# Kernel tuning notes

Measured on AMD Instinct MI355X. Metric: run time of the kernel, lower is better.

The kernel has to match this reference:

```python
import jax, jax.numpy as jnp
import numpy as np

TOP_K = 2
LORA_SCALE = 32.0 / 16.0  # alpha / r


def setup_inputs() -> dict:
    key = jax.random.key(0)
    ks = jax.random.split(key, 11)
    B, S, D, F, E, R = 4, 1024, 2048, 5632, 8, 16
    sd, sf = 1.0 / np.sqrt(D), 1.0 / np.sqrt(F)
    return {
        "x": jax.random.normal(ks[0], (B, S, D), jnp.float32),
        "gate_w": jax.random.normal(ks[1], (E, D), jnp.float32) * 0.02,
        "w1": jax.random.normal(ks[2], (F, D), jnp.float32) * sd,
        "w3": jax.random.normal(ks[3], (F, D), jnp.float32) * sd,
        "w2": jax.random.normal(ks[4], (D, F), jnp.float32) * sf,
        "a1": jax.random.normal(ks[5], (E, R, D), jnp.float32) * sd,
        "b1": jax.random.normal(ks[6], (E, F, R), jnp.float32) * 0.01,
        "a3": jax.random.normal(ks[7], (E, R, D), jnp.float32) * sd,
        "b3": jax.random.normal(ks[8], (E, F, R), jnp.float32) * 0.01,
        "a2": jax.random.normal(ks[9], (E, R, F), jnp.float32) * sf,
        "b2": jax.random.normal(ks[10], (E, D, R), jnp.float32) * 0.01,
    }


def reference(x, gate_w, w1, w3, w2, a1, b1, a3, b3, a2, b2):
    B, S, D = x.shape
    E = gate_w.shape[0]
    xf = x.reshape(B * S, D)                      # [N, D] tokens
    N = xf.shape[0]

    # Mixtral-style router: top-k over expert logits, softmax over selected.
    logits = xf @ gate_w.T                        # [N, E]
    top_w, top_i = jax.lax.top_k(logits, TOP_K)   # [N, k]
    routing = jax.nn.softmax(top_w, axis=-1)
    # Dense [N, E] routing-weight matrix (zero for unselected experts).
    w_full = jnp.zeros((N, E), x.dtype).at[jnp.arange(N)[:, None], top_i].add(routing)

    # Shared base up-projections computed once (same for every expert).
    base1 = xf @ w1.T                             # [N, F]
    base3 = xf @ w3.T                             # [N, F]

    def expert_step(acc, p):
        A1, B1, A3, B3, A2, B2, we = p            # we: [N] routing weight
        h1 = base1 + ((xf @ A1.T) @ B1.T) * LORA_SCALE
        h3 = base3 + ((xf @ A3.T) @ B3.T) * LORA_SCALE
        act = jax.nn.silu(h1) * h3                # SwiGLU, per-expert
        out = act @ w2.T + ((act @ A2.T) @ B2.T) * LORA_SCALE
        return acc + we[:, None] * out, None

    init = jnp.zeros((N, D), x.dtype)
    out, _ = jax.lax.scan(expert_step, init, (a1, b1, a3, b3, a2, b2, w_full.T))
    return out.reshape(B, S, D)
```

## Files before the change

### kernel.cpp

```cpp
#include <hip/hip_runtime.h>
#include <stdint.h>

#define NTOK 4096
#define DDIM 2048
#define FDIM 5632
#define NEXP 8
#define RLORA 16
#define TWOF 11264
#define BCOLS 11520
#define PADROWS 10240
#define LSCALE 2.0f

typedef __attribute__((ext_vector_type(4))) float f32x4;
typedef __attribute__((ext_vector_type(8))) short short8;
typedef unsigned short u16;

#define AS1 __attribute__((address_space(1)))
#define AS3 __attribute__((address_space(3)))

__device__ __forceinline__ float b2f(short s) {
  union { float f; unsigned u; } v;
  v.u = ((unsigned)(u16)s) << 16;
  return v.f;
}
__device__ __forceinline__ u16 f2b(float f) {
  union { float f; unsigned u; } v; v.f = f;
  unsigned r = v.u + 0x7fffu + ((v.u >> 16) & 1u);
  return (u16)(r >> 16);
}

__global__ __launch_bounds__(256) void cast_kernel(const float* __restrict__ src, u16* __restrict__ dst, int n4) {
  int stride = gridDim.x * 256;
  for (int i = blockIdx.x * 256 + threadIdx.x; i < n4; i += stride) {
    float4 v = reinterpret_cast<const float4*>(src)[i];
    ushort4 o;
    o.x = f2b(v.x); o.y = f2b(v.y); o.z = f2b(v.z); o.w = f2b(v.w);
    reinterpret_cast<ushort4*>(dst)[i] = o;
  }
}

__global__ __launch_bounds__(256) void cast_ball(const float* __restrict__ w1, const float* __restrict__ w3,
                                                 const float* __restrict__ a1, const float* __restrict__ a3,
                                                 u16* __restrict__ Ball) {
  const int n4 = BCOLS * DDIM / 4;
  int stride = gridDim.x * 256;
  for (int i = blockIdx.x * 256 + threadIdx.x; i < n4; i += stride) {
    int row = i >> 9;
    int c4 = i & 511;
    const float* src;
    if (row < FDIM)            src = w1 + (size_t)row * DDIM;
    else if (row < TWOF)       src = w3 + (size_t)(row - FDIM) * DDIM;
    else if (row < TWOF + 128) src = a1 + (size_t)(row - TWOF) * DDIM;
    else                       src = a3 + (size_t)(row - TWOF - 128) * DDIM;
    float4 v = reinterpret_cast<const float4*>(src)[c4];
    ushort4 o;
    o.x = f2b(v.x); o.y = f2b(v.y); o.z = f2b(v.z); o.w = f2b(v.w);
    reinterpret_cast<ushort4*>(Ball)[i] = o;
  }
}

__global__ __launch_bounds__(256) void router_cast(const float* __restrict__ x, const float* __restrict__ gw,
                                                   int2* __restrict__ tok_e, float2* __restrict__ tok_w,
                                                   u16* __restrict__ xb) {
  int tok = blockIdx.x;
  const float* xr = x + (size_t)tok * DDIM;
  int j0 = threadIdx.x * 8;
  float4 v0 = *reinterpret_cast<const float4*>(xr + j0);
  float4 v1 = *reinterpret_cast<const float4*>(xr + j0 + 4);
  float v[8] = {v0.x, v0.y, v0.z, v0.w, v1.x, v1.y, v1.z, v1.w};
  short8 ob;
#pragma unroll
  for (int j = 0; j < 8; ++j) ob[j] = (short)f2b(v[j]);
  *reinterpret_cast<short8*>(xb + (size_t)tok * DDIM + j0) = ob;
  float acc[NEXP];
#pragma unroll
  for (int e = 0; e < NEXP; ++e) {
    const float* gr = gw + e * DDIM + j0;
    float s = 0.f;
#pragma unroll
    for (int j = 0; j < 8; ++j) s += v[j] * gr[j];
    acc[e] = s;
  }
#pragma unroll
  for (int e = 0; e < NEXP; ++e) {
#pragma unroll
    for (int off = 32; off > 0; off >>= 1) acc[e] += __shfl_down(acc[e], off);
  }
  __shared__ float red[4][NEXP];
  int wid = threadIdx.x >> 6;
  int lane = threadIdx.x & 63;
  if (lane == 0) {
#pragma unroll
    for (int e = 0; e < NEXP; ++e) red[wid][e] = acc[e];
  }
  __syncthreads();
  if (threadIdx.x == 0) {
    float l[NEXP];
#pragma unroll
    for (int e = 0; e < NEXP; ++e) l[e] = red[0][e] + red[1][e] + red[2][e] + red[3][e];
    int i0 = 0;
#pragma unroll
    for (int e = 1; e < NEXP; ++e) if (l[e] > l[i0]) i0 = e;
    int i1 = (i0 == 0) ? 1 : 0;
#pragma unroll
    for (int e = 0; e < NEXP; ++e) if (e != i0 && e != i1 && l[e] > l[i1]) i1 = e;
    float ex = __expf(l[i1] - l[i0]);
    float w0 = 1.f / (1.f + ex);
    float w1v = ex / (1.f + ex);
    int2 ev; ev.x = i0; ev.y = i1;
    float2 wv; wv.x = w0; wv.y = w1v;
    tok_e[tok] = ev;
    tok_w[tok] = wv;
  }
}

__global__ __launch_bounds__(256) void build_pairs(const int2* __restrict__ tok_e,
                                                   int* __restrict__ pair_tok,
                                                   int* __restrict__ pair_k, int* __restrict__ poff) {
  __shared__ int cnt[NEXP];
  __shared__ int base[NEXP + 1];
  __shared__ int cur[NEXP];
  if (threadIdx.x < NEXP) cnt[threadIdx.x] = 0;
  __syncthreads();
  for (int t = threadIdx.x; t < NTOK; t += 256) {
    int2 ee = tok_e[t];
    atomicAdd(&cnt[ee.x], 1);
    atomicAdd(&cnt[ee.y], 1);
  }
  for (int i = threadIdx.x; i < PADROWS; i += 256) pair_tok[i] = -1;
  __syncthreads();
  if (threadIdx.x == 0) {
    int o = 0;
#pragma unroll
    for (int e = 0; e < NEXP; ++e) { base[e] = o; o += ((cnt[e] + 255) >> 8) << 8; }
    base[NEXP] = o;
  }
  __syncthreads();
  if (threadIdx.x < NEXP) cur[threadIdx.x] = base[threadIdx.x];
  __syncthreads();
  for (int t = threadIdx.x; t < NTOK; t += 256) {
    int2 ee = tok_e[t];
    int s0 = atomicAdd(&cur[ee.x], 1);
    pair_tok[s0] = t; pair_k[s0] = 0;
    int s1 = atomicAdd(&cur[ee.y], 1);
    pair_tok[s1] = t; pair_k[s1] = 1;
  }
  __syncthreads();
  if (threadIdx.x <= NEXP) poff[threadIdx.x] = base[threadIdx.x];
}

__device__ __forceinline__ void stage64(const u16* __restrict__ src, int ld, char* ldsb, int tid) {
#pragma unroll
  for (int h = 0; h < 4; ++h) {
    int q = h * 256 + tid;
    int r = q >> 3, g = q & 7;
    int gs = g ^ (r & 7);
    const char* s = (const char*)(src + (size_t)r * ld) + gs * 16;
    __builtin_amdgcn_global_load_lds((const AS1 void*)s, (AS3 void*)(ldsb + q * 16), 16, 0, 0);
  }
}

__device__ __forceinline__ void mm128(const u16* __restrict__ A, const u16* __restrict__ B,
                                      int lda, int ldb, int NT,
                                      char* lA, char* lB, int tid,
                                      int rowAb, int rowBb, int col0,
                                      f32x4 (&acc)[4][4]) {
  for (int t = 0; t < NT; ++t) {
    __syncthreads();
    stage64(A + (size_t)t * 64, lda, lA, tid);
    stage64(B + (size_t)t * 64, ldb, lB, tid);
    __syncthreads();
    short8 av[4], bv[4];
#pragma unroll
    for (int kh = 0; kh < 2; ++kh) {
      int col = col0 ^ (kh << 6);
#pragma unroll
      for (int i = 0; i < 4; ++i) {
        av[i] = *(const short8*)(lA + rowAb + i * 2048 + col);
        bv[i] = *(const short8*)(lB + rowBb + i * 2048 + col);
      }
#pragma unroll
      for (int i = 0; i < 4; ++i)
#pragma unroll
        for (int j = 0; j < 4; ++j)
          acc[i][j] = __builtin_amdgcn_mfma_f32_16x16x32_bf16(av[i], bv[j], acc[i][j], 0, 0, 0);
    }
  }
}

__global__ __launch_bounds__(256, 4) void gemm_base(const u16* __restrict__ xb, const u16* __restrict__ Ball,
                                                    u16* __restrict__ base13) {
  __shared__ char lA[16384];
  __shared__ char lB[16384];
  const int tid = threadIdx.x;
  const int lane = tid & 63, wid = tid >> 6;
  const int wr = wid >> 1, wc = wid & 1;
  const int lm = lane & 15, lg = lane >> 4;
  const int col0 = (lg << 4) ^ ((lm & 7) << 4);
  const int rowAb = (wr * 64 + lm) * 128;
  const int rowBb = (wc * 64 + lm) * 128;
  const int lq = (lane >> 4) << 2;
  int orig = blockIdx.x;
  int wgid = (orig & 7) * 360 + (orig >> 3);
  int mi = wgid & 31, nt = wgid >> 5;
  int m0 = mi << 7, n0 = nt << 7;
  f32x4 acc[4][4];
  f32x4 z = {0.f, 0.f, 0.f, 0.f};
#pragma unroll
  for (int i = 0; i < 4; ++i)
#pragma unroll
    for (int j = 0; j < 4; ++j) acc[i][j] = z;
  mm128(xb + (size_t)m0 * DDIM, Ball + (size_t)n0 * DDIM, DDIM, DDIM, DDIM / 64,
        lA, lB, tid, rowAb, rowBb, col0, acc);
#pragma unroll
  for (int i = 0; i < 4; ++i) {
#pragma unroll
    for (int n = 0; n < 4; ++n) {
      int col = n0 + wc * 64 + n * 16 + lm;
#pragma unroll
      for (int q = 0; q < 4; ++q) {
        int row = m0 + wr * 64 + i * 16 + lq + q;
        base13[(size_t)row * BCOLS + col] = f2b(acc[i][n][q]);
      }
    }
  }
}

__global__ __launch_bounds__(256) void act_kernel(const u16* __restrict__ base13,
                                                  const float* __restrict__ b1, const float* __restrict__ b3,
                                                  const int* __restrict__ pair_tok, const int* __restrict__ poff,
                                                  u16* __restrict__ act) {
  __shared__ float lb1[128 * 16];
  __shared__ float lb3[128 * 16];
  int f0 = blockIdx.x * 128;
  int r0 = blockIdx.y * 32;
  if (r0 >= poff[NEXP]) return;
  int e = 0;
  while (r0 >= poff[e + 1]) ++e;
  const float4* pb1 = reinterpret_cast<const float4*>(b1 + ((size_t)e * FDIM + f0) * RLORA);
  const float4* pb3 = reinterpret_cast<const float4*>(b3 + ((size_t)e * FDIM + f0) * RLORA);
  for (int i = threadIdx.x; i < 128 * 16 / 4; i += 256) {
    int r = i >> 2, c = i & 3;
    int cs = (c + (r >> 5)) & 3;
    *reinterpret_cast<float4*>(lb1 + r * 16 + cs * 4) = pb1[i];
    *reinterpret_cast<float4*>(lb3 + r * 16 + cs * 4) = pb3[i];
  }
  __syncthreads();
  int pr = r0 + (threadIdx.x >> 3);
  int fg = (threadIdx.x & 7) << 4;
  int tok = pair_tok[pr];
  if (tok < 0) return;
  const u16* bp = base13 + (size_t)tok * BCOLS;
  short8 x1a = *(const short8*)(bp + TWOF + e * 16);
  short8 x1b = *(const short8*)(bp + TWOF + e * 16 + 8);
  short8 x3a = *(const short8*)(bp + TWOF + NEXP * RLORA + e * 16);
  short8 x3b = *(const short8*)(bp + TWOF + NEXP * RLORA + e * 16 + 8);
  float xa1[16], xa3[16];
#pragma unroll
  for (int r = 0; r < 8; ++r) {
    xa1[r] = b2f(x1a[r]); xa1[r + 8] = b2f(x1b[r]);
    xa3[r] = b2f(x3a[r]); xa3[r + 8] = b2f(x3b[r]);
  }
  short8 h1a = *(const short8*)(bp + f0 + fg);
  short8 h1b = *(const short8*)(bp + f0 + fg + 8);
  short8 h3a = *(const short8*)(bp + FDIM + f0 + fg);
  short8 h3b = *(const short8*)(bp + FDIM + f0 + fg + 8);
  short8 o0, o1;
#pragma unroll
  for (int ii = 0; ii < 16; ++ii) {
    float hb1 = b2f(ii < 8 ? h1a[ii] : h1b[ii - 8]);
    float hb3 = b2f(ii < 8 ? h3a[ii] : h3b[ii - 8]);
    int row = fg + ii;
    int rot = row >> 5;
    const float* l1 = lb1 + row * 16;
    const float* l3 = lb3 + row * 16;
    float d1 = 0.f, d3 = 0.f;
#pragma unroll
    for (int c = 0; c < 4; ++c) {
      int cs = ((c + rot) & 3) << 2;
      float4 v1 = *reinterpret_cast<const float4*>(l1 + cs);
      float4 v3 = *reinterpret_cast<const float4*>(l3 + cs);
      d1 += xa1[4 * c + 0] * v1.x + xa1[4 * c + 1] * v1.y + xa1[4 * c + 2] * v1.z + xa1[4 * c + 3] * v1.w;
      d3 += xa3[4 * c + 0] * v3.x + xa3[4 * c + 1] * v3.y + xa3[4 * c + 2] * v3.z + xa3[4 * c + 3] * v3.w;
    }
    float h1 = hb1 + LSCALE * d1;
    float h3 = hb3 + LSCALE * d3;
    float s = h1 / (1.f + __expf(-h1));
    u16 ob = f2b(s * h3);
    if (ii < 8) o0[ii] = (short)ob; else o1[ii - 8] = (short)ob;
  }
  short8* dst = (short8*)(act + (size_t)pr * FDIM + f0 + fg);
  dst[0] = o0;
  dst[1] = o1;
}

__global__ __launch_bounds__(256) void ya2_kernel(const u16* __restrict__ act, const u16* __restrict__ a2b,
                                                  const int* __restrict__ poff, float* __restrict__ ya2) {
  __shared__ char lA[8192];
  __shared__ char lB[2048];
  int m0 = blockIdx.x * 64;
  if (m0 >= poff[NEXP]) return;
  int e = 0;
  while (m0 >= poff[e + 1]) ++e;
  int f0 = blockIdx.y * (FDIM / 2);
  const int tid = threadIdx.x;
  const int lane = tid & 63, w = tid >> 6;
  const int lm = lane & 15, lg = lane >> 4;
  const int col0 = (lg << 4) ^ ((lm & 7) << 4);
  const int rowAb = (w * 16 + lm) * 128;
  const int rowBb = lm * 128;
  const int lq = (lane >> 4) << 2;
  const u16* A = act + (size_t)m0 * FDIM + f0;
  const u16* B = a2b + (size_t)e * RLORA * FDIM + f0;
  f32x4 acc = {0.f, 0.f, 0.f, 0.f};
  for (int t = 0; t < FDIM / 128; ++t) {
    __syncthreads();
#pragma unroll
    for (int h = 0; h < 2; ++h) {
      int q = h * 256 + tid, r = q >> 3, g = q & 7, gs = g ^ (r & 7);
      const char* s = (const char*)(A + (size_t)t * 64 + (size_t)r * FDIM) + gs * 16;
      __builtin_amdgcn_global_load_lds((const AS1 void*)s, (AS3 void*)(lA + q * 16), 16, 0, 0);
    }
    if (tid < 128) {
      int q = tid, r = q >> 3, g = q & 7, gs = g ^ (r & 7);
      const char* s = (const char*)(B + (size_t)t * 64 + (size_t)r * FDIM) + gs * 16;
      __builtin_amdgcn_global_load_lds((const AS1 void*)s, (AS3 void*)(lB + q * 16), 16, 0, 0);
    }
    __syncthreads();
#pragma unroll
    for (int kh = 0; kh < 2; ++kh) {
      int col = col0 ^ (kh << 6);
      short8 av = *(const short8*)(lA + rowAb + col);
      short8 bv = *(const short8*)(lB + rowBb + col);
      acc = __builtin_amdgcn_mfma_f32_16x16x32_bf16(av, bv, acc, 0, 0, 0);
    }
  }
#pragma unroll
  for (int q = 0; q < 4; ++q)
    atomicAdd(&ya2[(size_t)(m0 + w * 16 + lq + q) * RLORA + lm], acc[q]);
}

__global__ __launch_bounds__(256, 4) void gemm_down(const u16* __restrict__ act, const u16* __restrict__ w2b,
                                                    const float* __restrict__ b2, const float* __restrict__ ya2,
                                                    const int* __restrict__ pair_tok, const int* __restrict__ pair_k,
                                                    const int* __restrict__ poff,
                                                    float* __restrict__ slots) {
  int orig = blockIdx.x;
  int wgid = (orig & 7) * 160 + (orig >> 3);
  int nt = wgid & 15;
  int miL = wgid >> 4;
  int mi = ((miL % 10) << 3) + (miL / 10);
  int m0 = mi << 7;
  if (m0 >= poff[NEXP]) return;
  int e = 0;
  while (m0 >= poff[e + 1]) ++e;
  int n0 = nt << 7;
  __shared__ char lA[16384];
  __shared__ char lB[16384];
  const int tid = threadIdx.x;
  const int lane = tid & 63, wid = tid >> 6;
  const int wr = wid >> 1, wc = wid & 1;
  const int lm = lane & 15, lg = lane >> 4;
  const int col0 = (lg << 4) ^ ((lm & 7) << 4);
  const int rowAb = (wr * 64 + lm) * 128;
  const int rowBb = (wc * 64 + lm) * 128;
  const int lq = (lane >> 4) << 2;
  f32x4 acc[4][4];
  f32x4 z = {0.f, 0.f, 0.f, 0.f};
#pragma unroll
  for (int i = 0; i < 4; ++i)
#pragma unroll
    for (int j = 0; j < 4; ++j) acc[i][j] = z;
  mm128(act + (size_t)m0 * FDIM, w2b + (size_t)n0 * FDIM, FDIM, FDIM, FDIM / 64,
        lA, lB, tid, rowAb, rowBb, col0, acc);
#pragma unroll
  for (int n = 0; n < 4; ++n) {
    int col = n0 + wc * 64 + n * 16 + lm;
    const float* b2p = b2 + ((size_t)e * DDIM + col) * RLORA;
    float b2v[16];
#pragma unroll
    for (int rr = 0; rr < 16; ++rr) b2v[rr] = b2p[rr];
#pragma unroll
    for (int i = 0; i < 4; ++i) {
#pragma unroll
      for (int q = 0; q < 4; ++q) {
        int pidx = m0 + wr * 64 + i * 16 + lq + q;
        int tok = pair_tok[pidx];
        if (tok < 0) continue;
        const float* yr = ya2 + (size_t)pidx * RLORA;
        float dot = 0.f;
#pragma unroll
        for (int rr = 0; rr < 16; ++rr) dot += yr[rr] * b2v[rr];
        slots[((size_t)tok * 2 + pair_k[pidx]) * DDIM + col] = acc[i][n][q] + LSCALE * dot;
      }
    }
  }
}

__global__ __launch_bounds__(256) void combine_kernel(const float4* __restrict__ slots,
                                                      const float2* __restrict__ tok_w,
                                                      float4* __restrict__ out) {
  const int n4 = NTOK * (DDIM / 4);
  int stride = gridDim.x * 256;
  for (int i = blockIdx.x * 256 + threadIdx.x; i < n4; i += stride) {
    int tok = i >> 9;
    int c = i & 511;
    float2 w = tok_w[tok];
    float4 v0 = slots[(size_t)(tok * 2) * 512 + c];
    float4 v1 = slots[(size_t)(tok * 2 + 1) * 512 + c];
    float4 o;
    o.x = w.x * v0.x + w.y * v1.x;
    o.y = w.x * v0.y + w.y * v1.y;
    o.z = w.x * v0.z + w.y * v1.z;
    o.w = w.x * v0.w + w.y * v1.w;
    out[i] = o;
  }
}

extern "C" void kernel_launch(void* const* d_in, const int* in_sizes, int n_in,
                              void* d_out, int out_size, void* d_ws, size_t ws_size,
                              hipStream_t stream) {
  (void)in_sizes; (void)n_in; (void)out_size; (void)ws_size;
  const float* x  = (const float*)d_in[0];
  const float* gw = (const float*)d_in[1];
  const float* w1 = (const float*)d_in[2];
  const float* w3 = (const float*)d_in[3];
  const float* w2 = (const float*)d_in[4];
  const float* a1 = (const float*)d_in[5];
  const float* b1 = (const float*)d_in[6];
  const float* a3 = (const float*)d_in[7];
  const float* b3 = (const float*)d_in[8];
  const float* a2 = (const float*)d_in[9];
  const float* b2 = (const float*)d_in[10];
  float* out = (float*)d_out;

  char* ws = (char*)d_ws;
  size_t off = 0;
  auto take = [&](size_t bytes) -> char* {
    char* p = ws + off;
    off += (bytes + 255) & ~(size_t)255;
    return p;
  };
  char* reg1 = take((size_t)NTOK * BCOLS * 2);
  u16* base13 = (u16*)reg1;
  float* slots = (float*)reg1;
  char* reg2 = take((size_t)PADROWS * FDIM * 2);
  u16* actb = (u16*)reg2;
  u16* xb = (u16*)reg2;
  u16* Ball = (u16*)(reg2 + (size_t)NTOK * DDIM * 2);
  u16* w2b = (u16*)take((size_t)DDIM * FDIM * 2);
  u16* a2b = (u16*)take((size_t)NEXP * RLORA * FDIM * 2);
  float* ya2 = (float*)take((size_t)PADROWS * RLORA * 4);
  int2* tok_e   = (int2*)take((size_t)NTOK * 8);
  float2* tok_w = (float2*)take((size_t)NTOK * 8);
  int* pair_tok = (int*)take((size_t)PADROWS * 4);
  int* pair_k   = (int*)take((size_t)PADROWS * 4);
  int* poff     = (int*)take(256);

  cast_ball<<<2048, 256, 0, stream>>>(w1, w3, a1, a3, Ball);
  cast_kernel<<<1024, 256, 0, stream>>>(w2, w2b, DDIM * FDIM / 4);
  cast_kernel<<<64, 256, 0, stream>>>(a2, a2b, NEXP * RLORA * FDIM / 4);
  router_cast<<<NTOK, 256, 0, stream>>>(x, gw, tok_e, tok_w, xb);
  build_pairs<<<1, 256, 0, stream>>>(tok_e, pair_tok, pair_k, poff);
  gemm_base<<<2880, 256, 0, stream>>>(xb, Ball, base13);
  dim3 g3(FDIM / 128, PADROWS / 32);
  act_kernel<<<g3, 256, 0, stream>>>(base13, b1, b3, pair_tok, poff, actb);
  hipMemsetAsync(ya2, 0, (size_t)PADROWS * RLORA * 4, stream);
  dim3 gy(PADROWS / 64, 2);
  ya2_kernel<<<gy, 256, 0, stream>>>(actb, a2b, poff, ya2);
  gemm_down<<<1280, 256, 0, stream>>>(actb, w2b, b2, ya2, pair_tok, pair_k, poff, slots);
  combine_kernel<<<2048, 256, 0, stream>>>((const float4*)slots, tok_w, (float4*)out);
}
```

Measured before the change: 776.7 us.

## Fuse SwiGLU activation into base up-projection GEMM epilogue with interleaved w1/w3 tiles

Interleaves w1 and w3 rows in 64-row blocks so each 128-column tile of the base GEMM holds matching h1 and h3 columns. Adds an LDS exchange so the epilogue computes the LoRA correction, SiLU and product in place and writes bf16 activations straight to both expert slots. This removes the bf16 base13 round trip and the separate act_kernel. The x·A1/A3 LoRA projections move to a new per-expert xa_kernel, and B1/B3 are transposed to bf16. In exchange the epilogue runs on only half the waves, does scattered global writes, and uses more LDS per block, which may lower occupancy.

```diff
diff --git a/kernel.cpp b/kernel.cpp
--- a/kernel.cpp
+++ b/kernel.cpp
@@ -7,7 +7,6 @@
 #define NEXP 8
 #define RLORA 16
 #define TWOF 11264
-#define BCOLS 11520
 #define PADROWS 10240
 #define LSCALE 2.0f
 
@@ -39,23 +38,51 @@
   }
 }
 
-__global__ __launch_bounds__(256) void cast_ball(const float* __restrict__ w1, const float* __restrict__ w3,
-                                                 const float* __restrict__ a1, const float* __restrict__ a3,
-                                                 u16* __restrict__ Ball) {
-  const int n4 = BCOLS * DDIM / 4;
+__global__ __launch_bounds__(256) void cast_ball_i(const float* __restrict__ w1, const float* __restrict__ w3,
+                                                   u16* __restrict__ Ball) {
+  const int n4 = TWOF * DDIM / 4;
   int stride = gridDim.x * 256;
   for (int i = blockIdx.x * 256 + threadIdx.x; i < n4; i += stride) {
     int row = i >> 9;
     int c4 = i & 511;
-    const float* src;
-    if (row < FDIM)            src = w1 + (size_t)row * DDIM;
-    else if (row < TWOF)       src = w3 + (size_t)(row - FDIM) * DDIM;
-    else if (row < TWOF + 128) src = a1 + (size_t)(row - TWOF) * DDIM;
-    else                       src = a3 + (size_t)(row - TWOF - 128) * DDIM;
+    int blk = row >> 7, w = row & 127;
+    const float* src = (w < 64) ? (w1 + (size_t)(blk * 64 + w) * DDIM)
+                                : (w3 + (size_t)(blk * 64 + w - 64) * DDIM);
     float4 v = reinterpret_cast<const float4*>(src)[c4];
     ushort4 o;
     o.x = f2b(v.x); o.y = f2b(v.y); o.z = f2b(v.z); o.w = f2b(v.w);
     reinterpret_cast<ushort4*>(Ball)[i] = o;
+  }
+}
+
+__global__ __launch_bounds__(256) void cast_a13(const float* __restrict__ a1, const float* __restrict__ a3,
+                                                u16* __restrict__ a13b) {
+  const int n4 = 256 * DDIM / 4;
+  int stride = gridDim.x * 256;
+  for (int i = blockIdx.x * 256 + threadIdx.x; i < n4; i += stride) {
+    int row = i >> 9, c4 = i & 511;
+    int e = row >> 5, w = row & 31;
+    const float* src = (w < 16) ? (a1 + (size_t)(e * 16 + w) * DDIM)
+                                : (a3 + (size_t)(e * 16 + w - 16) * DDIM);
+    float4 v = reinterpret_cast<const float4*>(src)[c4];
+    ushort4 o;
+    o.x = f2b(v.x); o.y = f2b(v.y); o.z = f2b(v.z); o.w = f2b(v.w);
+    reinterpret_cast<ushort4*>(a13b)[i] = o;
+  }
+}
+
+__global__ __launch_bounds__(256) void cast_b13t(const float* __restrict__ b1, const float* __restrict__ b3,
+                                                 u16* __restrict__ b1t, u16* __restrict__ b3t) {
+  int e = blockIdx.y;
+  const int n4 = FDIM * RLORA / 4;
+  for (int i = blockIdx.x * 256 + threadIdx.x; i < n4; i += gridDim.x * 256) {
+    int f = i >> 2, r4 = (i & 3) << 2;
+    float4 v = *reinterpret_cast<const float4*>(b1 + ((size_t)e * FDIM + f) * RLORA + r4);
+    ushort4 o; o.x = f2b(v.x); o.y = f2b(v.y); o.z = f2b(v.z); o.w = f2b(v.w);
+    *reinterpret_cast<ushort4*>(b1t + ((size_t)f * NEXP + e) * RLORA + r4) = o;
+    v = *reinterpret_cast<const float4*>(b3 + ((size_t)e * FDIM + f) * RLORA + r4);
+    ushort4 o3; o3.x = f2b(v.x); o3.y = f2b(v.y); o3.z = f2b(v.z); o3.w = f2b(v.w);
+    *reinterpret_cast<ushort4*>(b3t + ((size_t)f * NEXP + e) * RLORA + r4) = o3;
   }
 }
 
@@ -116,7 +143,8 @@
 
 __global__ __launch_bounds__(256) void build_pairs(const int2* __restrict__ tok_e,
                                                    int* __restrict__ pair_tok,
-                                                   int* __restrict__ pair_k, int* __restrict__ poff) {
+                                                   int* __restrict__ pair_k, int* __restrict__ poff,
+                                                   int2* __restrict__ slot2) {
   __shared__ int cnt[NEXP];
   __shared__ int base[NEXP + 1];
   __shared__ int cur[NEXP];
@@ -144,6 +172,8 @@
     pair_tok[s0] = t; pair_k[s0] = 0;
     int s1 = atomicAdd(&cur[ee.y], 1);
     pair_tok[s1] = t; pair_k[s1] = 1;
+    int2 sv; sv.x = s0; sv.y = s1;
+    slot2[t] = sv;
   }
   __syncthreads();
   if (threadIdx.x <= NEXP) poff[threadIdx.x] = base[threadIdx.x];
@@ -188,10 +218,72 @@
   }
 }
 
-__global__ __launch_bounds__(256, 4) void gemm_base(const u16* __restrict__ xb, const u16* __restrict__ Ball,
-                                                    u16* __restrict__ base13) {
-  __shared__ char lA[16384];
-  __shared__ char lB[16384];
+__global__ __launch_bounds__(256) void xa_kernel(const u16* __restrict__ xb, const u16* __restrict__ a13b,
+                                                 const int* __restrict__ pair_tok, const int* __restrict__ poff,
+                                                 float* __restrict__ xa) {
+  __shared__ char lA[8192];
+  __shared__ char lB[4096];
+  int m0 = blockIdx.x * 64;
+  if (m0 >= poff[NEXP]) return;
+  int e = 0;
+  while (m0 >= poff[e + 1]) ++e;
+  const int tid = threadIdx.x;
+  const int lane = tid & 63, w = tid >> 6;
+  const int lm = lane & 15, lg = lane >> 4;
+  const int col0 = (lg << 4) ^ ((lm & 7) << 4);
+  const int rowAb = (w * 16 + lm) * 128;
+  const int rowB1 = lm * 128;
+  const int rowB3 = (16 + lm) * 128;
+  const int lq = lg << 2;
+  int r0 = tid >> 3;
+  int t0 = pair_tok[m0 + r0];      if (t0 < 0) t0 = 0;
+  int t1 = pair_tok[m0 + 32 + r0]; if (t1 < 0) t1 = 0;
+  const u16* B = a13b + (size_t)e * 32 * DDIM;
+  f32x4 acc0 = {0.f, 0.f, 0.f, 0.f}, acc1 = {0.f, 0.f, 0.f, 0.f};
+  for (int t = 0; t < DDIM / 64; ++t) {
+    __syncthreads();
+    {
+      int g = tid & 7, gs = g ^ (r0 & 7);
+      const char* s = (const char*)(xb + (size_t)t0 * DDIM + t * 64) + gs * 16;
+      __builtin_amdgcn_global_load_lds((const AS1 void*)s, (AS3 void*)(lA + tid * 16), 16, 0, 0);
+    }
+    {
+      int r = 32 + r0, g = tid & 7, gs = g ^ (r & 7);
+      const char* s = (const char*)(xb + (size_t)t1 * DDIM + t * 64) + gs * 16;
+      __builtin_amdgcn_global_load_lds((const AS1 void*)s, (AS3 void*)(lA + 4096 + tid * 16), 16, 0, 0);
+    }
+    {
+      int r = tid >> 3, g = tid & 7, gs = g ^ (r & 7);
+      const char* s = (const char*)(B + (size_t)r * DDIM + t * 64) + gs * 16;
+      __builtin_amdgcn_global_load_lds((const AS1 void*)s, (AS3 void*)(lB + tid * 16), 16, 0, 0);
+    }
+    __syncthreads();
+#pragma unroll
+    for (int kh = 0; kh < 2; ++kh) {
+      int col = col0 ^ (kh << 6);
+      short8 av = *(const short8*)(lA + rowAb + col);
+      short8 b1v = *(const short8*)(lB + rowB1 + col);
+      short8 b3v = *(const short8*)(lB + rowB3 + col);
+      acc0 = __builtin_amdgcn_mfma_f32_16x16x32_bf16(av, b1v, acc0, 0, 0, 0);
+      acc1 = __builtin_amdgcn_mfma_f32_16x16x32_bf16(av, b3v, acc1, 0, 0, 0);
+    }
+  }
+#pragma unroll
+  for (int q = 0; q < 4; ++q) {
+    size_t base = (size_t)(m0 + w * 16 + lq + q) * 32;
+    xa[base + lm] = acc0[q];
+    xa[base + 16 + lm] = acc1[q];
+  }
+}
+
+__global__ __launch_bounds__(256, 4) void gemm_fused(const u16* __restrict__ xb, const u16* __restrict__ Ball,
+                                                     const u16* __restrict__ b1t, const u16* __restrict__ b3t,
+                                                     const float* __restrict__ xa,
+                                                     const int2* __restrict__ slot2, const int2* __restrict__ tok_e,
+                                                     u16* __restrict__ act) {
+  __shared__ char lds[34816];
+  char* lA = lds;
+  char* lB = lds + 16384;
   const int tid = threadIdx.x;
   const int lane = tid & 63, wid = tid >> 6;
   const int wr = wid >> 1, wc = wid & 1;
@@ -199,99 +291,73 @@
   const int col0 = (lg << 4) ^ ((lm & 7) << 4);
   const int rowAb = (wr * 64 + lm) * 128;
   const int rowBb = (wc * 64 + lm) * 128;
-  const int lq = (lane >> 4) << 2;
+  const int lq = lg << 2;
   int orig = blockIdx.x;
-  int wgid = (orig & 7) * 360 + (orig >> 3);
+  int wgid = (orig & 7) * 352 + (orig >> 3);
   int mi = wgid & 31, nt = wgid >> 5;
-  int m0 = mi << 7, n0 = nt << 7;
+  int m0 = mi << 7;
   f32x4 acc[4][4];
   f32x4 z = {0.f, 0.f, 0.f, 0.f};
 #pragma unroll
   for (int i = 0; i < 4; ++i)
 #pragma unroll
     for (int j = 0; j < 4; ++j) acc[i][j] = z;
-  mm128(xb + (size_t)m0 * DDIM, Ball + (size_t)n0 * DDIM, DDIM, DDIM, DDIM / 64,
+  mm128(xb + (size_t)m0 * DDIM, Ball + (size_t)(nt << 7) * DDIM, DDIM, DDIM, DDIM / 64,
         lA, lB, tid, rowAb, rowBb, col0, acc);
-#pragma unroll
-  for (int i = 0; i < 4; ++i) {
-#pragma unroll
-    for (int n = 0; n < 4; ++n) {
-      int col = n0 + wc * 64 + n * 16 + lm;
-#pragma unroll
+  __syncthreads();
+  float* xch = (float*)lds;
+  if (wc == 1) {
+#pragma unroll
+    for (int i = 0; i < 4; ++i)
+#pragma unroll
+      for (int n = 0; n < 4; ++n)
+#pragma unroll
+        for (int q = 0; q < 4; ++q)
+          xch[(wr * 64 + i * 16 + lq + q) * 68 + n * 16 + lm] = acc[i][n][q];
+  }
+  __syncthreads();
+  if (wc == 0) {
+    int fb = nt << 6;
+    for (int i = 0; i < 4; ++i) {
       for (int q = 0; q < 4; ++q) {
-        int row = m0 + wr * 64 + i * 16 + lq + q;
-        base13[(size_t)row * BCOLS + col] = f2b(acc[i][n][q]);
+        int rl = wr * 64 + i * 16 + lq + q;
+        int tok = m0 + rl;
+        int2 sl = slot2[tok];
+        int2 ee = tok_e[tok];
+        for (int k = 0; k < 2; ++k) {
+          int s = k ? sl.y : sl.x;
+          int e = k ? ee.y : ee.x;
+          const float* xp = xa + (size_t)s * 32;
+          float x1v[16], x3v[16];
+#pragma unroll
+          for (int c = 0; c < 4; ++c) {
+            float4 v1 = *reinterpret_cast<const float4*>(xp + c * 4);
+            float4 v3 = *reinterpret_cast<const float4*>(xp + 16 + c * 4);
+            x1v[4 * c] = v1.x; x1v[4 * c + 1] = v1.y; x1v[4 * c + 2] = v1.z; x1v[4 * c + 3] = v1.w;
+            x3v[4 * c] = v3.x; x3v[4 * c + 1] = v3.y; x3v[4 * c + 2] = v3.z; x3v[4 * c + 3] = v3.w;
+          }
+#pragma unroll
+          for (int n = 0; n < 4; ++n) {
+            int fl = n * 16 + lm;
+            int f = fb + fl;
+            const short8* pb1 = (const short8*)(b1t + ((size_t)f * NEXP + e) * RLORA);
+            const short8* pb3 = (const short8*)(b3t + ((size_t)f * NEXP + e) * RLORA);
+            short8 b1a = pb1[0], b1b = pb1[1], b3a = pb3[0], b3b = pb3[1];
+            float l1 = 0.f, l3 = 0.f;
+#pragma unroll
+            for (int r = 0; r < 8; ++r) {
+              l1 += x1v[r] * b2f(b1a[r]) + x1v[r + 8] * b2f(b1b[r]);
+              l3 += x3v[r] * b2f(b3a[r]) + x3v[r + 8] * b2f(b3b[r]);
+            }
+            float H1 = acc[i][n][q] + LSCALE * l1;
+            float H3 = xch[rl * 68 + fl] + LSCALE * l3;
+            float sv = H1 / (1.f + __expf(-H1));
+            act[(size_t)s * FDIM + f] = f2b(sv * H3);
+          }
+        }
       }
     }
   }
-}
-
-__global__ __launch_bounds__(256) void act_kernel(const u16* __restrict__ base13,
-                                                  const float* __restrict__ b1, const float* __restrict__ b3,
-                                                  const int* __restrict__ pair_tok, const int* __restrict__ poff,
-                                                  u16* __restrict__ act) {
-  __shared__ float lb1[128 * 16];
-  __shared__ float lb3[128 * 16];
-  int f0 = blockIdx.x * 128;
-  int r0 = blockIdx.y * 32;
-  if (r0 >= poff[NEXP]) return;
-  int e = 0;
-  while (r0 >= poff[e + 1]) ++e;
-  const float4* pb1 = reinterpret_cast<const float4*>(b1 + ((size_t)e * FDIM + f0) * RLORA);
-  const float4* pb3 = reinterpret_cast<const float4*>(b3 + ((size_t)e * FDIM + f0) * RLORA);
-  for (int i = threadIdx.x; i < 128 * 16 / 4; i += 256) {
-    int r = i >> 2, c = i & 3;
-    int cs = (c + (r >> 5)) & 3;
-    *reinterpret_cast<float4*>(lb1 + r * 16 + cs * 4) = pb1[i];
-    *reinterpret_cast<float4*>(lb3 + r * 16 + cs * 4) = pb3[i];
-  }
-  __syncthreads();
-  int pr = r0 + (threadIdx.x >> 3);
-  int fg = (threadIdx.x & 7) << 4;
-  int tok = pair_tok[pr];
-  if (tok < 0) return;
-  const u16* bp = base13 + (size_t)tok * BCOLS;
-  short8 x1a = *(const short8*)(bp + TWOF + e * 16);
-  short8 x1b = *(const short8*)(bp + TWOF + e * 16 + 8);
-  short8 x3a = *(const short8*)(bp + TWOF + NEXP * RLORA + e * 16);
-  short8 x3b = *(const short8*)(bp + TWOF + NEXP * RLORA + e * 16 + 8);
-  float xa1[16], xa3[16];
-#pragma unroll
-  for (int r = 0; r < 8; ++r) {
-    xa1[r] = b2f(x1a[r]); xa1[r + 8] = b2f(x1b[r]);
-    xa3[r] = b2f(x3a[r]); xa3[r + 8] = b2f(x3b[r]);
-  }
-  short8 h1a = *(const short8*)(bp + f0 + fg);
-  short8 h1b = *(const short8*)(bp + f0 + fg + 8);
-  short8 h3a = *(const short8*)(bp + FDIM + f0 + fg);
-  short8 h3b = *(const short8*)(bp + FDIM + f0 + fg + 8);
-  short8 o0, o1;
-#pragma unroll
-  for (int ii = 0; ii < 16; ++ii) {
-    float hb1 = b2f(ii < 8 ? h1a[ii] : h1b[ii - 8]);
-    float hb3 = b2f(ii < 8 ? h3a[ii] : h3b[ii - 8]);
-    int row = fg + ii;
-    int rot = row >> 5;
-    const float* l1 = lb1 + row * 16;
-    const float* l3 = lb3 + row * 16;
-    float d1 = 0.f, d3 = 0.f;
-#pragma unroll
-    for (int c = 0; c < 4; ++c) {
-      int cs = ((c + rot) & 3) << 2;
-      float4 v1 = *reinterpret_cast<const float4*>(l1 + cs);
-      float4 v3 = *reinterpret_cast<const float4*>(l3 + cs);
-      d1 += xa1[4 * c + 0] * v1.x + xa1[4 * c + 1] * v1.y + xa1[4 * c + 2] * v1.z + xa1[4 * c + 3] * v1.w;
-      d3 += xa3[4 * c + 0] * v3.x + xa3[4 * c + 1] * v3.y + xa3[4 * c + 2] * v3.z + xa3[4 * c + 3] * v3.w;
-    }
-    float h1 = hb1 + LSCALE * d1;
-    float h3 = hb3 + LSCALE * d3;
-    float s = h1 / (1.f + __expf(-h1));
-    u16 ob = f2b(s * h3);
-    if (ii < 8) o0[ii] = (short)ob; else o1[ii - 8] = (short)ob;
-  }
-  short8* dst = (short8*)(act + (size_t)pr * FDIM + f0 + fg);
-  dst[0] = o0;
-  dst[1] = o1;
 }
 
 __global__ __launch_bounds__(256) void ya2_kernel(const u16* __restrict__ act, const u16* __restrict__ a2b,
@@ -309,7 +375,7 @@
   const int col0 = (lg << 4) ^ ((lm & 7) << 4);
   const int rowAb = (w * 16 + lm) * 128;
   const int rowBb = lm * 128;
-  const int lq = (lane >> 4) << 2;
+  const int lq = lg << 2;
   const u16* A = act + (size_t)m0 * FDIM + f0;
   const u16* B = a2b + (size_t)e * RLORA * FDIM + f0;
   f32x4 acc = {0.f, 0.f, 0.f, 0.f};
@@ -364,7 +430,7 @@
   const int col0 = (lg << 4) ^ ((lm & 7) << 4);
   const int rowAb = (wr * 64 + lm) * 128;
   const int rowBb = (wc * 64 + lm) * 128;
-  const int lq = (lane >> 4) << 2;
+  const int lq = lg << 2;
   f32x4 acc[4][4];
   f32x4 z = {0.f, 0.f, 0.f, 0.f};
 #pragma unroll
@@ -441,30 +507,35 @@
     off += (bytes + 255) & ~(size_t)255;
     return p;
   };
-  char* reg1 = take((size_t)NTOK * BCOLS * 2);
-  u16* base13 = (u16*)reg1;
-  float* slots = (float*)reg1;
-  char* reg2 = take((size_t)PADROWS * FDIM * 2);
-  u16* actb = (u16*)reg2;
-  u16* xb = (u16*)reg2;
-  u16* Ball = (u16*)(reg2 + (size_t)NTOK * DDIM * 2);
-  u16* w2b = (u16*)take((size_t)DDIM * FDIM * 2);
-  u16* a2b = (u16*)take((size_t)NEXP * RLORA * FDIM * 2);
+  char* regA = take((size_t)NTOK * 2 * DDIM * 4);
+  u16* xb = (u16*)regA;
+  u16* Ball = (u16*)(regA + (size_t)NTOK * DDIM * 2);
+  float* slots = (float*)regA;
+  u16* actb = (u16*)take((size_t)PADROWS * FDIM * 2);
+  u16* w2b  = (u16*)take((size_t)DDIM * FDIM * 2);
+  u16* a2b  = (u16*)take((size_t)NEXP * RLORA * FDIM * 2);
+  u16* a13b = (u16*)take((size_t)NEXP * 32 * DDIM * 2);
+  u16* b1t  = (u16*)take((size_t)FDIM * NEXP * RLORA * 2);
+  u16* b3t  = (u16*)take((size_t)FDIM * NEXP * RLORA * 2);
   float* ya2 = (float*)take((size_t)PADROWS * RLORA * 4);
+  float* xa  = (float*)take((size_t)PADROWS * 32 * 4);
   int2* tok_e   = (int2*)take((size_t)NTOK * 8);
   float2* tok_w = (float2*)take((size_t)NTOK * 8);
+  int2* slot2   = (int2*)take((size_t)NTOK * 8);
   int* pair_tok = (int*)take((size_t)PADROWS * 4);
   int* pair_k   = (int*)take((size_t)PADROWS * 4);
   int* poff     = (int*)take(256);
 
-  cast_ball<<<2048, 256, 0, stream>>>(w1, w3, a1, a3, Ball);
+  cast_ball_i<<<2048, 256, 0, stream>>>(w1, w3, Ball);
+  cast_a13<<<64, 256, 0, stream>>>(a1, a3, a13b);
   cast_kernel<<<1024, 256, 0, stream>>>(w2, w2b, DDIM * FDIM / 4);
   cast_kernel<<<64, 256, 0, stream>>>(a2, a2b, NEXP * RLORA * FDIM / 4);
+  dim3 gb(88, 8);
+  cast_b13t<<<gb, 256, 0, stream>>>(b1, b3, b1t, b3t);
   router_cast<<<NTOK, 256, 0, stream>>>(x, gw, tok_e, tok_w, xb);
-  build_pairs<<<1, 256, 0, stream>>>(tok_e, pair_tok, pair_k, poff);
-  gemm_base<<<2880, 256, 0, stream>>>(xb, Ball, base13);
-  dim3 g3(FDIM / 128, PADROWS / 32);
-  act_kernel<<<g3, 256, 0, stream>>>(base13, b1, b3, pair_tok, poff, actb);
+  build_pairs<<<1, 256, 0, stream>>>(tok_e, pair_tok, pair_k, poff, slot2);
+  xa_kernel<<<PADROWS / 64, 256, 0, stream>>>(xb, a13b, pair_tok, poff, xa);
+  gemm_fused<<<2816, 256, 0, stream>>>(xb, Ball, b1t, b3t, xa, slot2, tok_e, actb);
   hipMemsetAsync(ya2, 0, (size_t)PADROWS * RLORA * 4, stream);
   dim3 gy(PADROWS / 64, 2);
   ya2_kernel<<<gy, 256, 0, stream>>>(actb, a2b, poff, ya2);
```

New measurement: 1.861 ms. 140% more time.
